# Kernel optimization log

Measured on AMD Instinct MI355X. Metric: run time of the kernel, lower is better.

## Reference

```python
import jax, jax.numpy as jnp
import numpy as np

V, D, U, B, S = 100000, 256, 512, 64, 128


def setup_inputs() -> dict:
    key = jax.random.key(0)
    k0, k1, k2, k3 = jax.random.split(key, 4)
    x = jax.random.randint(k0, (B, S), 0, V)  # token ids
    hidden = jnp.zeros((B, U), jnp.float32)   # initialize_hidden_state()
    embedding = jax.random.normal(k1, (V, D), jnp.float32) * 0.02
    kernel = jax.random.normal(k2, (D, 3 * U), jnp.float32) * (1.0 / np.sqrt(D))
    recurrent_kernel = jax.random.normal(k3, (U, 3 * U), jnp.float32) * (1.0 / np.sqrt(U))
    bias = jnp.zeros((2, 3 * U), jnp.float32)  # [input_bias, recurrent_bias] (reset_after=True)
    return {"x": x, "hidden": hidden, "embedding": embedding,
            "kernel": kernel, "recurrent_kernel": recurrent_kernel, "bias": bias}


def reference(x, hidden, embedding, kernel, recurrent_kernel, bias):
    # Vectorized replacement of the token-by-token get_embedding gather.
    emb = embedding[x]                      # [B, S, D]
    b_in, b_rec = bias[0], bias[1]
    # Precompute all input projections in one GEMM: [B, S, 3U]
    xp = jnp.einsum('bsd,dk->bsk', emb, kernel) + b_in

    def step(h, xt):
        rp = h @ recurrent_kernel + b_rec           # [B, 3U]
        xz, xr, xh = jnp.split(xt, 3, axis=-1)
        rz, rr, rh = jnp.split(rp, 3, axis=-1)
        z = jax.nn.sigmoid(xz + rz)
        r = jax.nn.sigmoid(xr + rr)
        hh = jnp.tanh(xh + r * rh)                  # reset_after=True form
        hn = z * h + (1.0 - z) * hh
        return hn, hn

    state, outs = jax.lax.scan(step, hidden, jnp.swapaxes(xp, 0, 1))
    output = jnp.swapaxes(outs, 0, 1)               # [B, S, U]
    return output, state
```

## Files before the change

kernel.cpp:

```cpp
#include <hip/hip_runtime.h>
#include <hip/hip_bf16.h>

#define NB   64
#define NS   128
#define ND   256
#define NU   512
#define N3   1536

typedef __attribute__((ext_vector_type(4))) float  f32x4;
typedef __attribute__((ext_vector_type(8))) short  s16x8;
typedef unsigned long long u64;
typedef unsigned int       u32;
typedef unsigned short     u16;

__device__ __forceinline__ u16 f2bf(float v) {
  unsigned u = __builtin_bit_cast(unsigned, v);
  u += 0x7fffu + ((u >> 16) & 1u);
  return (u16)(u >> 16);
}

__global__ void init_kernel(const float* __restrict__ hidden,
                            u16* __restrict__ hx,
                            u32* __restrict__ cnt) {
  const int b = blockIdx.x, u = threadIdx.x;
  hx[b * NU + u] = f2bf(hidden[b * NU + u]);
  const int i = b * NU + u;
  if (i < 4 * NS) cnt[i] = 0u;
}

__global__ __launch_bounds__(256) void xproj_kernel(
    const int* __restrict__ x, const float* __restrict__ emb,
    const float* __restrict__ W, const float* __restrict__ bias,
    float* __restrict__ xp) {
  __shared__ float As[32][68];
  __shared__ float Bs[32][68];
  __shared__ int tok[64];
  const int tid = threadIdx.x;
  const int m0 = blockIdx.y * 64;
  const int n0 = blockIdx.x * 64;
  if (tid < 64) tok[tid] = x[m0 + tid];
  __syncthreads();
  const int tx = tid & 15, ty = tid >> 4;
  float acc[4][4] = {};
  for (int k0 = 0; k0 < ND; k0 += 32) {
    {
      const int m = tid & 63, kq = tid >> 6;
      const float* src = emb + (size_t)tok[m] * ND + k0 + kq * 8;
      const float4 v0 = *(const float4*)(src);
      const float4 v1 = *(const float4*)(src + 4);
      As[kq*8+0][m] = v0.x; As[kq*8+1][m] = v0.y;
      As[kq*8+2][m] = v0.z; As[kq*8+3][m] = v0.w;
      As[kq*8+4][m] = v1.x; As[kq*8+5][m] = v1.y;
      As[kq*8+6][m] = v1.z; As[kq*8+7][m] = v1.w;
    }
    {
      const int n = (tid & 15) * 4, k = tid >> 4;
      *(float4*)&Bs[k][n]    = *(const float4*)&W[(size_t)(k0 + k) * N3 + n0 + n];
      *(float4*)&Bs[k+16][n] = *(const float4*)&W[(size_t)(k0 + k + 16) * N3 + n0 + n];
    }
    __syncthreads();
    #pragma unroll
    for (int kk = 0; kk < 32; ++kk) {
      const float4 b4 = *(const float4*)&Bs[kk][tx * 4];
      float a[4];
      #pragma unroll
      for (int i = 0; i < 4; ++i) a[i] = As[kk][ty * 4 + i];
      #pragma unroll
      for (int i = 0; i < 4; ++i) {
        acc[i][0] += a[i] * b4.x;
        acc[i][1] += a[i] * b4.y;
        acc[i][2] += a[i] * b4.z;
        acc[i][3] += a[i] * b4.w;
      }
    }
    __syncthreads();
  }
  #pragma unroll
  for (int i = 0; i < 4; ++i) {
    const size_t row = (size_t)(m0 + ty * 4 + i) * N3 + n0 + tx * 4;
    float4 o;
    o.x = acc[i][0] + bias[n0 + tx*4 + 0];
    o.y = acc[i][1] + bias[n0 + tx*4 + 1];
    o.z = acc[i][2] + bias[n0 + tx*4 + 2];
    o.w = acc[i][3] + bias[n0 + tx*4 + 3];
    *(float4*)&xp[row] = o;
  }
}

__global__ __launch_bounds__(128) void gru_scan_kernel(
    const float* __restrict__ xp, const float* __restrict__ hidden,
    const float* __restrict__ R, const float* __restrict__ bias,
    float* __restrict__ out, u16* __restrict__ hx,
    u32* __restrict__ cnt) {
  __shared__ u16 Rt[96][520];

  const int bid = blockIdx.x;
  const int g   = bid >> 4;
  const int u0  = (bid & 15) * 32;
  const int tid = threadIdx.x;
  const int lane = tid & 63;
  const int wv   = tid >> 6;

  for (int idx = tid; idx < 512 * 128; idx += 128) {
    const int k = idx >> 7, c = idx & 127;
    if (c < 96) {
      const int wc = c / 48, r = c % 48, j = r >> 4, cuu = r & 15;
      Rt[c][k] = f2bf(R[(size_t)k * N3 + (j << 9) + u0 + (wc << 4) + cuu]);
    }
  }
  __syncthreads();

  const int ar  = lane & 15;
  const int kg  = lane >> 4;
  const int cu  = lane & 15;
  const int myu = u0 + (wv << 4) + cu;
  const int drow = kg << 2;
  const int cb  = wv * 48 + cu;

  const float bz = bias[N3 + myu];
  const float br = bias[N3 + 512 + myu];
  const float bh = bias[N3 + 1024 + myu];

  float hr[4];
  #pragma unroll
  for (int i = 0; i < 4; ++i)
    hr[i] = hidden[(size_t)((g << 4) + drow + i) * NU + myu];

  for (int t = 0; t < NS; ++t) {
    float xg0[4], xg1[4], xg2[4];
    #pragma unroll
    for (int i = 0; i < 4; ++i) {
      const float* q = xp + ((size_t)(((g << 4) + drow + i) * NS) + t) * N3 + myu;
      xg0[i] = q[0]; xg1[i] = q[512]; xg2[i] = q[1024];
    }

    if (t > 0) {
      const u32* c = &cnt[g * NS + (t - 1)];
      while (__hip_atomic_load(c, __ATOMIC_RELAXED,
                               __HIP_MEMORY_SCOPE_AGENT) != 32u) {}
      asm volatile("" ::: "memory");
    }

    u64 alo[16], ahi[16];
    u64* hrow = (u64*)(hx + ((size_t)t * NB + (g << 4) + ar) * NU);
    #pragma unroll
    for (int ks = 0; ks < 16; ++ks) {
      const int qi = (ks << 3) + (kg << 1);
      alo[ks] = __hip_atomic_load(&hrow[qi],     __ATOMIC_RELAXED, __HIP_MEMORY_SCOPE_AGENT);
      ahi[ks] = __hip_atomic_load(&hrow[qi + 1], __ATOMIC_RELAXED, __HIP_MEMORY_SCOPE_AGENT);
    }

    f32x4 a0 = {0.f,0.f,0.f,0.f}, a1 = a0, a2 = a0;
    #pragma unroll
    for (int ks = 0; ks < 16; ++ks) {
      union { u64 q[2]; s16x8 v; } af;
      af.q[0] = alo[ks]; af.q[1] = ahi[ks];
      const int kb = (ks << 5) + (kg << 3);
      a0 = __builtin_amdgcn_mfma_f32_16x16x32_bf16(af.v, *(const s16x8*)&Rt[cb][kb],      a0, 0,0,0);
      a1 = __builtin_amdgcn_mfma_f32_16x16x32_bf16(af.v, *(const s16x8*)&Rt[cb + 16][kb], a1, 0,0,0);
      a2 = __builtin_amdgcn_mfma_f32_16x16x32_bf16(af.v, *(const s16x8*)&Rt[cb + 32][kb], a2, 0,0,0);
    }

    #pragma unroll
    for (int i = 0; i < 4; ++i) {
      const float z = 1.f / (1.f + __expf(-(xg0[i] + a0[i] + bz)));
      const float r = 1.f / (1.f + __expf(-(xg1[i] + a1[i] + br)));
      const float e = __expf(2.f * (xg2[i] + r * (a2[i] + bh)));
      const float hh = (e - 1.f) / (e + 1.f);
      hr[i] = z * hr[i] + (1.f - z) * hh;
    }

    if (t < NS - 1) {
      #pragma unroll
      for (int i = 0; i < 4; ++i)
        __hip_atomic_store(&hx[((size_t)(t + 1) * NB + (g << 4) + drow + i) * NU + myu],
                           f2bf(hr[i]), __ATOMIC_RELAXED, __HIP_MEMORY_SCOPE_AGENT);
      asm volatile("s_waitcnt vmcnt(0)" ::: "memory");
      if (lane == 0)
        __hip_atomic_fetch_add(&cnt[g * NS + t], 1u,
                               __ATOMIC_RELAXED, __HIP_MEMORY_SCOPE_AGENT);
    }

    #pragma unroll
    for (int i = 0; i < 4; ++i)
      out[((size_t)((g << 4) + drow + i) * NS + t) * NU + myu] = hr[i];
    if (t == NS - 1) {
      #pragma unroll
      for (int i = 0; i < 4; ++i)
        out[(size_t)NB * NS * NU + (size_t)((g << 4) + drow + i) * NU + myu] = hr[i];
    }
  }
}

extern "C" void kernel_launch(void* const* d_in, const int* in_sizes, int n_in,
                              void* d_out, int out_size, void* d_ws, size_t ws_size,
                              hipStream_t stream) {
  const int*   x      = (const int*)d_in[0];
  const float* hidden = (const float*)d_in[1];
  const float* emb    = (const float*)d_in[2];
  const float* W      = (const float*)d_in[3];
  const float* R      = (const float*)d_in[4];
  const float* bias   = (const float*)d_in[5];
  float* out = (float*)d_out;

  char* ws = (char*)d_ws;
  float* xp  = (float*)ws;
  u16*   hx  = (u16*)(ws + 50331648);
  u32*   cnt = (u32*)(ws + 50331648 + 8454144);

  init_kernel<<<NB, NU, 0, stream>>>(hidden, hx, cnt);
  dim3 gA(N3 / 64, (NB * NS) / 64);
  xproj_kernel<<<gA, 256, 0, stream>>>(x, emb, W, bias, xp);
  gru_scan_kernel<<<64, 128, 0, stream>>>(xp, hidden, R, bias, out, hx, cnt);
}
```

Before: 773.0 us.

## Replace counter barrier with sentinel-filled hidden buffer polling

Each slot of the per-step bf16 hidden buffer is pre-filled with a NaN sentinel. The scan kernel now polls its hidden-state loads until no element carries the sentinel bit, so the atomic counter, its spin-wait and the vmcnt drain before each increment are all removed. This turns a two-hop handshake (data store, then counter) into a single data-as-flag wait. In exchange the init kernel must write the entire 127-step buffer, and correctness depends on real bf16 values never having bit 14 set, which holds only for magnitudes below 2. The tanh expression is also rewritten in a slightly cheaper form.

```diff
diff --git a/kernel.cpp b/kernel.cpp
--- a/kernel.cpp
+++ b/kernel.cpp
@@ -13,19 +13,22 @@
 typedef unsigned int       u32;
 typedef unsigned short     u16;
 
+#define SENT64  0x7FC07FC07FC07FC0ull
+#define BIT14x4 0x4000400040004000ull
+
 __device__ __forceinline__ u16 f2bf(float v) {
   unsigned u = __builtin_bit_cast(unsigned, v);
   u += 0x7fffu + ((u >> 16) & 1u);
   return (u16)(u >> 16);
 }
 
-__global__ void init_kernel(const float* __restrict__ hidden,
-                            u16* __restrict__ hx,
-                            u32* __restrict__ cnt) {
-  const int b = blockIdx.x, u = threadIdx.x;
-  hx[b * NU + u] = f2bf(hidden[b * NU + u]);
-  const int i = b * NU + u;
-  if (i < 4 * NS) cnt[i] = 0u;
+__global__ __launch_bounds__(512) void init_kernel(const float* __restrict__ hidden,
+                                                   u16* __restrict__ hx) {
+  const int tid = blockIdx.x * 512 + threadIdx.x;
+  hx[tid] = f2bf(hidden[tid]);
+  u64* fill = (u64*)(hx + NB * NU);
+  const int n = 127 * NB * NU / 4;
+  for (int i = tid; i < n; i += NB * NU) fill[i] = SENT64;
 }
 
 __global__ __launch_bounds__(256) void xproj_kernel(
@@ -90,8 +93,7 @@
 __global__ __launch_bounds__(128) void gru_scan_kernel(
     const float* __restrict__ xp, const float* __restrict__ hidden,
     const float* __restrict__ R, const float* __restrict__ bias,
-    float* __restrict__ out, u16* __restrict__ hx,
-    u32* __restrict__ cnt) {
+    float* __restrict__ out, u16* __restrict__ hx) {
   __shared__ u16 Rt[96][520];
 
   const int bid = blockIdx.x;
@@ -134,21 +136,23 @@
       xg0[i] = q[0]; xg1[i] = q[512]; xg2[i] = q[1024];
     }
 
-    if (t > 0) {
-      const u32* c = &cnt[g * NS + (t - 1)];
-      while (__hip_atomic_load(c, __ATOMIC_RELAXED,
-                               __HIP_MEMORY_SCOPE_AGENT) != 32u) {}
-      asm volatile("" ::: "memory");
-    }
-
     u64 alo[16], ahi[16];
-    u64* hrow = (u64*)(hx + ((size_t)t * NB + (g << 4) + ar) * NU);
-    #pragma unroll
-    for (int ks = 0; ks < 16; ++ks) {
-      const int qi = (ks << 3) + (kg << 1);
-      alo[ks] = __hip_atomic_load(&hrow[qi],     __ATOMIC_RELAXED, __HIP_MEMORY_SCOPE_AGENT);
-      ahi[ks] = __hip_atomic_load(&hrow[qi + 1], __ATOMIC_RELAXED, __HIP_MEMORY_SCOPE_AGENT);
-    }
+    const u64* hrow = (const u64*)(hx + ((size_t)t * NB + (g << 4) + ar) * NU);
+    int ok = 0;
+    do {
+      if (!ok) {
+        #pragma unroll
+        for (int ks = 0; ks < 16; ++ks) {
+          const int qi = (ks << 3) + (kg << 1);
+          alo[ks] = __hip_atomic_load(&hrow[qi],     __ATOMIC_RELAXED, __HIP_MEMORY_SCOPE_AGENT);
+          ahi[ks] = __hip_atomic_load(&hrow[qi + 1], __ATOMIC_RELAXED, __HIP_MEMORY_SCOPE_AGENT);
+        }
+        u64 m = 0;
+        #pragma unroll
+        for (int ks = 0; ks < 16; ++ks) m |= alo[ks] | ahi[ks];
+        ok = ((m & BIT14x4) == 0) ? 1 : 0;
+      }
+    } while (!__all(ok));
 
     f32x4 a0 = {0.f,0.f,0.f,0.f}, a1 = a0, a2 = a0;
     #pragma unroll
@@ -166,7 +170,7 @@
       const float z = 1.f / (1.f + __expf(-(xg0[i] + a0[i] + bz)));
       const float r = 1.f / (1.f + __expf(-(xg1[i] + a1[i] + br)));
       const float e = __expf(2.f * (xg2[i] + r * (a2[i] + bh)));
-      const float hh = (e - 1.f) / (e + 1.f);
+      const float hh = 1.f - 2.f / (e + 1.f);
       hr[i] = z * hr[i] + (1.f - z) * hh;
     }
 
@@ -175,10 +179,6 @@
       for (int i = 0; i < 4; ++i)
         __hip_atomic_store(&hx[((size_t)(t + 1) * NB + (g << 4) + drow + i) * NU + myu],
                            f2bf(hr[i]), __ATOMIC_RELAXED, __HIP_MEMORY_SCOPE_AGENT);
-      asm volatile("s_waitcnt vmcnt(0)" ::: "memory");
-      if (lane == 0)
-        __hip_atomic_fetch_add(&cnt[g * NS + t], 1u,
-                               __ATOMIC_RELAXED, __HIP_MEMORY_SCOPE_AGENT);
     }
 
     #pragma unroll
@@ -206,10 +206,9 @@
   char* ws = (char*)d_ws;
   float* xp  = (float*)ws;
   u16*   hx  = (u16*)(ws + 50331648);
-  u32*   cnt = (u32*)(ws + 50331648 + 8454144);
-
-  init_kernel<<<NB, NU, 0, stream>>>(hidden, hx, cnt);
+
+  init_kernel<<<NB, NU, 0, stream>>>(hidden, hx);
   dim3 gA(N3 / 64, (NB * NS) / 64);
   xproj_kernel<<<gA, 256, 0, stream>>>(x, emb, W, bias, xp);
-  gru_scan_kernel<<<64, 128, 0, stream>>>(xp, hidden, R, bias, out, hx, cnt);
-}
+  gru_scan_kernel<<<64, 128, 0, stream>>>(xp, hidden, R, bias, out, hx);
+}
```

Result: slower. 825.7 us (+6.8%).

## Poll hidden-state data directly using NaN sentinels instead of waiting on counters

Applied to the files above, without the earlier changes.

The init kernel now fills the per-step hidden-state buffer with a bf16 NaN sentinel. Each scan step first reads the previous hidden row directly and checks bit 14 of every element, for up to four rounds. If no sentinel remains it skips the atomic counter spin and the separate reload. This removes one round trip of latency from the cross-block dependency chain. In exchange, init writes an extra ~8 MB and the check assumes real hidden values stay below magnitude 2. The tanh is also rewritten as 1-2/(e+1), which avoids inf/inf and saves a subtraction.

```diff
diff --git a/kernel.cpp b/kernel.cpp
--- a/kernel.cpp
+++ b/kernel.cpp
@@ -6,6 +6,7 @@
 #define ND   256
 #define NU   512
 #define N3   1536
+#define KPROBE 4
 
 typedef __attribute__((ext_vector_type(4))) float  f32x4;
 typedef __attribute__((ext_vector_type(8))) short  s16x8;
@@ -13,19 +14,24 @@
 typedef unsigned int       u32;
 typedef unsigned short     u16;
 
+#define SENT64  0x7FC07FC07FC07FC0ull
+#define BIT14x4 0x4000400040004000ull
+
 __device__ __forceinline__ u16 f2bf(float v) {
   unsigned u = __builtin_bit_cast(unsigned, v);
   u += 0x7fffu + ((u >> 16) & 1u);
   return (u16)(u >> 16);
 }
 
-__global__ void init_kernel(const float* __restrict__ hidden,
-                            u16* __restrict__ hx,
-                            u32* __restrict__ cnt) {
-  const int b = blockIdx.x, u = threadIdx.x;
-  hx[b * NU + u] = f2bf(hidden[b * NU + u]);
-  const int i = b * NU + u;
-  if (i < 4 * NS) cnt[i] = 0u;
+__global__ __launch_bounds__(512) void init_kernel(const float* __restrict__ hidden,
+                                                   u16* __restrict__ hx,
+                                                   u32* __restrict__ cnt) {
+  const int tid = blockIdx.x * 512 + threadIdx.x;
+  hx[tid] = f2bf(hidden[tid]);
+  u64* fill = (u64*)(hx + NB * NU);
+  const int n = 127 * NB * NU / 4;
+  for (int i = tid; i < n; i += NB * NU) fill[i] = SENT64;
+  if (tid < 4 * NS) cnt[tid] = 0u;
 }
 
 __global__ __launch_bounds__(256) void xproj_kernel(
@@ -134,20 +140,32 @@
       xg0[i] = q[0]; xg1[i] = q[512]; xg2[i] = q[1024];
     }
 
-    if (t > 0) {
+    u64 alo[16], ahi[16];
+    const u64* hrow = (const u64*)(hx + ((size_t)t * NB + (g << 4) + ar) * NU);
+    int done = 0;
+    for (int rnd = 0; rnd < KPROBE && !done; ++rnd) {
+      #pragma unroll
+      for (int ks = 0; ks < 16; ++ks) {
+        const int qi = (ks << 3) + (kg << 1);
+        alo[ks] = __hip_atomic_load(&hrow[qi],     __ATOMIC_RELAXED, __HIP_MEMORY_SCOPE_AGENT);
+        ahi[ks] = __hip_atomic_load(&hrow[qi + 1], __ATOMIC_RELAXED, __HIP_MEMORY_SCOPE_AGENT);
+      }
+      u64 m = 0;
+      #pragma unroll
+      for (int ks = 0; ks < 16; ++ks) m |= alo[ks] | ahi[ks];
+      done = __all(((m & BIT14x4) == 0) ? 1 : 0) ? 1 : 0;
+    }
+    if (!done && t > 0) {
       const u32* c = &cnt[g * NS + (t - 1)];
       while (__hip_atomic_load(c, __ATOMIC_RELAXED,
                                __HIP_MEMORY_SCOPE_AGENT) != 32u) {}
       asm volatile("" ::: "memory");
-    }
-
-    u64 alo[16], ahi[16];
-    u64* hrow = (u64*)(hx + ((size_t)t * NB + (g << 4) + ar) * NU);
-    #pragma unroll
-    for (int ks = 0; ks < 16; ++ks) {
-      const int qi = (ks << 3) + (kg << 1);
-      alo[ks] = __hip_atomic_load(&hrow[qi],     __ATOMIC_RELAXED, __HIP_MEMORY_SCOPE_AGENT);
-      ahi[ks] = __hip_atomic_load(&hrow[qi + 1], __ATOMIC_RELAXED, __HIP_MEMORY_SCOPE_AGENT);
+      #pragma unroll
+      for (int ks = 0; ks < 16; ++ks) {
+        const int qi = (ks << 3) + (kg << 1);
+        alo[ks] = __hip_atomic_load(&hrow[qi],     __ATOMIC_RELAXED, __HIP_MEMORY_SCOPE_AGENT);
+        ahi[ks] = __hip_atomic_load(&hrow[qi + 1], __ATOMIC_RELAXED, __HIP_MEMORY_SCOPE_AGENT);
+      }
     }
 
     f32x4 a0 = {0.f,0.f,0.f,0.f}, a1 = a0, a2 = a0;
@@ -166,7 +184,7 @@
       const float z = 1.f / (1.f + __expf(-(xg0[i] + a0[i] + bz)));
       const float r = 1.f / (1.f + __expf(-(xg1[i] + a1[i] + br)));
       const float e = __expf(2.f * (xg2[i] + r * (a2[i] + bh)));
-      const float hh = (e - 1.f) / (e + 1.f);
+      const float hh = 1.f - 2.f / (e + 1.f);
       hr[i] = z * hr[i] + (1.f - z) * hh;
     }
 
@@ -206,7 +224,7 @@
   char* ws = (char*)d_ws;
   float* xp  = (float*)ws;
   u16*   hx  = (u16*)(ws + 50331648);
-  u32*   cnt = (u32*)(ws + 50331648 + 8454144);
+  u32*   cnt = (u32*)(ws + 50331648 + 8388608);
 
   init_kernel<<<NB, NU, 0, stream>>>(hidden, hx, cnt);
   dim3 gA(N3 / 64, (NB * NS) / 64);
```

Result: slower. 849.6 us (+9.9%).
